# Optimization experiments

Measured on AMD Instinct MI355X. Metric: run time of the kernel, lower is better.

## Reference

```python
import jax, jax.numpy as jnp
import numpy as np

# LoFTR coarse-matching config (eval path, no padding masks)
THR = 0.2
BORDER_RM = 2
TEMP = 0.1
H0C, W0C = 60, 80  # L = 4800
H1C, W1C = 60, 80  # S = 4800
N, C = 2, 256


def _border_valid(h, w, bd):
    # flat [h*w] bool, False within bd of any border of the (h, w) grid
    hi = jnp.arange(h)
    wi = jnp.arange(w)
    vh = (hi >= bd) & (hi < h - bd)
    vw = (wi >= bd) & (wi < w - bd)
    return (vh[:, None] & vw[None, :]).reshape(-1)


def setup_inputs() -> dict:
    key = jax.random.key(0)
    k0, k1 = jax.random.split(key)
    feat_c0 = jax.random.normal(k0, (N, H0C * W0C, C), dtype=jnp.float32)
    feat_c1 = jax.random.normal(k1, (N, H1C * W1C, C), dtype=jnp.float32)
    return {"feat_c0": feat_c0, "feat_c1": feat_c1}


def reference(feat_c0, feat_c1):
    c = feat_c0.shape[-1]
    inv_sqrt_c = 1.0 / (float(c) ** 0.5)
    f0 = feat_c0 * inv_sqrt_c
    f1 = feat_c1 * inv_sqrt_c
    # [N, L, S] similarity
    sim = jnp.einsum('nlc,nsc->nls', f0, f1) / TEMP
    # dual softmax
    conf = jax.nn.softmax(sim, axis=1) * jax.nn.softmax(sim, axis=2)
    # threshold + border removal
    mask = conf > THR
    valid0 = _border_valid(H0C, W0C, BORDER_RM)  # [L]
    valid1 = _border_valid(H1C, W1C, BORDER_RM)  # [S]
    mask = mask & valid0[None, :, None] & valid1[None, None, :]
    # mutual nearest neighbour
    mask = mask \
        & (conf == jnp.max(conf, axis=2, keepdims=True)) \
        & (conf == jnp.max(conf, axis=1, keepdims=True))
    return conf, mask
```

## Files before the change

kernel.cpp:

```cpp
#include <hip/hip_runtime.h>
#include <hip/hip_bf16.h>
#include <cstdint>

static constexpr int   Nb = 2;
static constexpr int   L  = 4800;
static constexpr int   S  = 4800;
static constexpr int   C  = 256;
static constexpr float THR = 0.2f;
static constexpr float SIM_SCALE = 1.0f / 25.6f;
static constexpr unsigned CAND_CAP = 65536;

using f32x4  = __attribute__((ext_vector_type(4))) float;
using bf16x8 = __attribute__((ext_vector_type(8))) short;
using u32x4  = __attribute__((ext_vector_type(4))) unsigned int;

__device__ inline unsigned short bf16_rne(float x) {
    unsigned u = __float_as_uint(x);
    unsigned r = (u + 0x7FFFu + ((u >> 16) & 1u)) >> 16;
    return (unsigned short)r;
}

__global__ __launch_bounds__(256) void cvt_bf16(const float* __restrict__ in0,
                                                const float* __restrict__ in1,
                                                unsigned short* __restrict__ out0,
                                                unsigned short* __restrict__ out1,
                                                int n8,
                                                unsigned* __restrict__ stats, int nStats) {
    if (blockIdx.y == 0) {
        int si = blockIdx.x * 256 + threadIdx.x;
        if (si < nStats) stats[si] = 0u;
    }
    const float* in = blockIdx.y ? in1 : in0;
    unsigned short* out = blockIdx.y ? out1 : out0;
    int i = blockIdx.x * 256 + threadIdx.x;
    if (i >= n8) return;
    f32x4 a = *(const f32x4*)(in + (size_t)i * 8);
    f32x4 b = *(const f32x4*)(in + (size_t)i * 8 + 4);
    union { unsigned short us[8]; u32x4 v; } r;
#pragma unroll
    for (int j = 0; j < 4; j++) r.us[j] = bf16_rne(a[j]);
#pragma unroll
    for (int j = 0; j < 4; j++) r.us[4 + j] = bf16_rne(b[j]);
    *(u32x4*)(out + (size_t)i * 8) = r.v;
}

__device__ inline bool border_ok(int idx) {
    int h = idx / 80, w = idx % 80;
    return (h >= 2) & (h < 58) & (w >= 2) & (w < 78);
}

#define BM 96
#define BN 192
#define BK 64

static constexpr int NWG   = (L / BM) * (S / BN) * Nb;
static constexpr int TILE_X = S / BN;
static constexpr int TILES_PER_N = (L / BM) * TILE_X;
static constexpr int XQ = NWG / 8;
static constexpr int XR = NWG % 8;

__device__ inline void gload16(const void* g, void* l) {
    __builtin_amdgcn_global_load_lds(
        (const __attribute__((address_space(1))) unsigned int*)g,
        (__attribute__((address_space(3))) unsigned int*)l, 16, 0, 0);
}

template <int MODE>
__global__ __launch_bounds__(256) void gemm_pass(
    const unsigned short* __restrict__ Abf,
    const unsigned short* __restrict__ Bbf,
    float* __restrict__ rowSum,
    float* __restrict__ colSum,
    float* __restrict__ conf,
    float* __restrict__ mask,
    unsigned* __restrict__ rowMax,
    unsigned* __restrict__ colMax,
    unsigned* __restrict__ cnt,
    unsigned* __restrict__ cand)
{
    __shared__ unsigned short As[BM * BK];
    __shared__ unsigned short Bs[BN * BK];

    const int orig = blockIdx.x;
    const int xcd  = orig & 7;
    const int idx  = orig >> 3;
    const int wgid = (xcd < XR ? xcd * (XQ + 1) : XR * (XQ + 1) + (xcd - XR) * XQ) + idx;
    const int n    = wgid / TILES_PER_N;
    const int rem  = wgid % TILES_PER_N;
    const int rb   = (rem / TILE_X) * BM;
    const int cb   = (rem % TILE_X) * BN;

    const int t  = threadIdx.x;
    const int lane = t & 63;
    const int wid  = t >> 6;
    const int wr = wid >> 1, wc = wid & 1;

    const unsigned short* Ag = Abf + ((size_t)n * L + rb) * C;
    const unsigned short* Bg = Bbf + ((size_t)n * S + cb) * C;

    f32x4 acc[3][6] = {};

    for (int kt = 0; kt < C; kt += BK) {
#pragma unroll
        for (int i = 0; i < 3; i++) {
            int ix = wid * 192 + i * 64 + lane;
            int row = ix >> 3;
            int src = ((ix & 7) ^ (row & 7)) * 8 + kt;
            gload16(Ag + (size_t)row * C + src, &As[(wid * 192 + i * 64) * 8]);
        }
#pragma unroll
        for (int i = 0; i < 6; i++) {
            int ix = wid * 384 + i * 64 + lane;
            int row = ix >> 3;
            int src = ((ix & 7) ^ (row & 7)) * 8 + kt;
            gload16(Bg + (size_t)row * C + src, &Bs[(wid * 384 + i * 64) * 8]);
        }
        __syncthreads();

#pragma unroll
        for (int kk = 0; kk < 2; kk++) {
            bf16x8 a[3], b[6];
            const int kElem = kk * 32 + (lane >> 4) * 8;
#pragma unroll
            for (int f = 0; f < 3; f++) {
                int ra = wr * 48 + f * 16 + (lane & 15);
                a[f] = *(const bf16x8*)&As[ra * 64 + (kElem ^ ((ra & 7) << 3))];
            }
#pragma unroll
            for (int f = 0; f < 6; f++) {
                int rbi = wc * 96 + f * 16 + (lane & 15);
                b[f] = *(const bf16x8*)&Bs[rbi * 64 + (kElem ^ ((rbi & 7) << 3))];
            }
#pragma unroll
            for (int fi = 0; fi < 3; fi++)
#pragma unroll
                for (int fj = 0; fj < 6; fj++)
                    acc[fi][fj] = __builtin_amdgcn_mfma_f32_16x16x32_bf16(
                        b[fj], a[fi], acc[fi][fj], 0, 0, 0);
        }
        __syncthreads();
    }

    const int rowBase = rb + wr * 48;
    const int colBase = cb + wc * 96;

    if constexpr (MODE == 0) {
        float csum[6][4] = {};
#pragma unroll
        for (int fi = 0; fi < 3; fi++) {
            const int l = rowBase + fi * 16 + (lane & 15);
            float rsum = 0.f;
#pragma unroll
            for (int fj = 0; fj < 6; fj++) {
#pragma unroll
                for (int r = 0; r < 4; r++) {
                    float e = __expf(acc[fi][fj][r] * SIM_SCALE);
                    rsum += e;
                    csum[fj][r] += e;
                }
            }
            rsum += __shfl_xor(rsum, 16);
            rsum += __shfl_xor(rsum, 32);
            if (lane < 16)
                atomicAdd(&rowSum[(size_t)n * L + l], rsum);
        }
#pragma unroll
        for (int fj = 0; fj < 6; fj++)
#pragma unroll
            for (int r = 0; r < 4; r++) {
                float v = csum[fj][r];
                v += __shfl_xor(v, 1);
                v += __shfl_xor(v, 2);
                v += __shfl_xor(v, 4);
                v += __shfl_xor(v, 8);
                if ((lane & 15) == 0)
                    atomicAdd(&colSum[(size_t)n * S + colBase + fj * 16 + ((lane >> 4) << 2) + r], v);
            }
        const f32x4 zero4 = {0.f, 0.f, 0.f, 0.f};
        const size_t mbase = (size_t)wgid * 18432;
#pragma unroll
        for (int i = 0; i < 18; i++)
            *(f32x4*)&mask[mbase + ((size_t)i * 256 + t) * 4] = zero4;
    } else {
        f32x4 invD1[6];
#pragma unroll
        for (int fj = 0; fj < 6; fj++) {
            const int s0 = colBase + fj * 16 + ((lane >> 4) << 2);
            f32x4 d1 = *(const f32x4*)&colSum[(size_t)n * S + s0];
#pragma unroll
            for (int j = 0; j < 4; j++) invD1[fj][j] = 1.0f / d1[j];
        }
        float cmax[6][4] = {};

#pragma unroll
        for (int fi = 0; fi < 3; fi++) {
            const int l = rowBase + fi * 16 + (lane & 15);
            const float invD2 = 1.0f / rowSum[(size_t)n * L + l];
            const bool bl = border_ok(l);
            float rmax = 0.f;
#pragma unroll
            for (int fj = 0; fj < 6; fj++) {
                const int s0 = colBase + fj * 16 + ((lane >> 4) << 2);
                f32x4 cv;
#pragma unroll
                for (int r = 0; r < 4; r++) {
                    float e = __expf(acc[fi][fj][r] * SIM_SCALE);
                    float c = e * e * invD1[fj][r] * invD2;
                    cv[r] = c;
                    rmax = fmaxf(rmax, c);
                    cmax[fj][r] = fmaxf(cmax[fj][r], c);
                    if (c > THR) {
                        int s = s0 + r;
                        if (bl && border_ok(s)) {
                            unsigned pos = atomicAdd(cnt, 1u);
                            if (pos < CAND_CAP) {
                                cand[2 * pos]     = (unsigned)(((size_t)n * L + l) * S + s);
                                cand[2 * pos + 1] = __float_as_uint(c);
                            }
                        }
                    }
                }
                *(f32x4*)&conf[((size_t)n * L + l) * S + s0] = cv;
            }
            rmax = fmaxf(rmax, __shfl_xor(rmax, 16));
            rmax = fmaxf(rmax, __shfl_xor(rmax, 32));
            if (lane < 16)
                atomicMax(&rowMax[(size_t)n * L + l], __float_as_uint(rmax));
        }
#pragma unroll
        for (int fj = 0; fj < 6; fj++)
#pragma unroll
            for (int r = 0; r < 4; r++) {
                float v = cmax[fj][r];
                v = fmaxf(v, __shfl_xor(v, 1));
                v = fmaxf(v, __shfl_xor(v, 2));
                v = fmaxf(v, __shfl_xor(v, 4));
                v = fmaxf(v, __shfl_xor(v, 8));
                if ((lane & 15) == 0)
                    atomicMax(&colMax[(size_t)n * S + colBase + fj * 16 + ((lane >> 4) << 2) + r],
                              __float_as_uint(v));
            }
    }
}

__global__ __launch_bounds__(256) void mask_scatter(
    const unsigned* __restrict__ cnt,
    const unsigned* __restrict__ cand,
    const unsigned* __restrict__ rowMax,
    const unsigned* __restrict__ colMax,
    float* __restrict__ mask)
{
    unsigned nc = *cnt;
    if (nc > CAND_CAP) nc = CAND_CAP;
    for (unsigned i = blockIdx.x * 256 + threadIdx.x; i < nc; i += gridDim.x * 256) {
        unsigned flat = cand[2 * i];
        unsigned bits = cand[2 * i + 1];
        unsigned row = flat / S;
        unsigned s   = flat % S;
        unsigned n   = row / L;
        if (bits == rowMax[row] && bits == colMax[n * S + s])
            mask[flat] = 1.0f;
    }
}

extern "C" void kernel_launch(void* const* d_in, const int* in_sizes, int n_in,
                              void* d_out, int out_size, void* d_ws, size_t ws_size,
                              hipStream_t stream) {
    (void)in_sizes; (void)n_in; (void)out_size; (void)ws_size;
    const float* f0 = (const float*)d_in[0];
    const float* f1 = (const float*)d_in[1];

    float* conf = (float*)d_out;
    float* mask = conf + (size_t)Nb * L * S;

    unsigned short* Abf = (unsigned short*)d_ws;
    unsigned short* Bbf = Abf + (size_t)Nb * L * C;
    float* rowSum = (float*)(Bbf + (size_t)Nb * S * C);
    float* colSum = rowSum + (size_t)Nb * L;
    unsigned* rowMax = (unsigned*)(colSum + (size_t)Nb * S);
    unsigned* colMax = rowMax + (size_t)Nb * L;
    unsigned* cnt    = colMax + (size_t)Nb * S;
    unsigned* cand   = cnt + 2;

    const int nStats = 2 * (Nb * L + Nb * S) + 1;
    const int n8 = Nb * L * C / 8;
    cvt_bf16<<<dim3((n8 + 255) / 256, 2), 256, 0, stream>>>(f0, f1, Abf, Bbf, n8,
                                                            (unsigned*)rowSum, nStats);

    gemm_pass<0><<<NWG, 256, 0, stream>>>(Abf, Bbf, rowSum, colSum,
                                          nullptr, mask, nullptr, nullptr, nullptr, nullptr);
    gemm_pass<1><<<NWG, 256, 0, stream>>>(Abf, Bbf, rowSum, colSum,
                                          conf, nullptr, rowMax, colMax, cnt, cand);

    mask_scatter<<<32, 256, 0, stream>>>(cnt, cand, rowMax, colMax, mask);
}
```

Baseline: 161.9 us.

## Keep full-K A tile resident in LDS and process five column tiles per block

Each workgroup now loads its whole 96x256 A row tile into LDS once and then loops over five consecutive 192-wide B column tiles, reusing A instead of reloading it per tile. The grid shrinks by a factor of five and launch bounds request two blocks per CU. The aim is to cut A global loads and per-block launch overhead. The cost is more LDS per block, fewer blocks to spread across CUs (a possible tail imbalance), and longer serial work per block with no overlap between tiles.

```diff
diff --git a/kernel.cpp b/kernel.cpp
--- a/kernel.cpp
+++ b/kernel.cpp
@@ -16,8 +16,7 @@
 
 __device__ inline unsigned short bf16_rne(float x) {
     unsigned u = __float_as_uint(x);
-    unsigned r = (u + 0x7FFFu + ((u >> 16) & 1u)) >> 16;
-    return (unsigned short)r;
+    return (unsigned short)((u + 0x7FFFu + ((u >> 16) & 1u)) >> 16);
 }
 
 __global__ __launch_bounds__(256) void cvt_bf16(const float* __restrict__ in0,
@@ -53,11 +52,14 @@
 #define BN 192
 #define BK 64
 
-static constexpr int NWG   = (L / BM) * (S / BN) * Nb;
+static constexpr int NT     = C / BK;
+static constexpr int TPBLK  = 5;
 static constexpr int TILE_X = S / BN;
 static constexpr int TILES_PER_N = (L / BM) * TILE_X;
-static constexpr int XQ = NWG / 8;
-static constexpr int XR = NWG % 8;
+static constexpr int NTILES = TILES_PER_N * Nb;
+static constexpr int NBLK   = NTILES / TPBLK;
+static constexpr int XQ = NBLK / 8;
+static constexpr int XR = NBLK % 8;
 
 __device__ inline void gload16(const void* g, void* l) {
     __builtin_amdgcn_global_load_lds(
@@ -66,7 +68,7 @@
 }
 
 template <int MODE>
-__global__ __launch_bounds__(256) void gemm_pass(
+__global__ __launch_bounds__(256, 2) void gemm_pass(
     const unsigned short* __restrict__ Abf,
     const unsigned short* __restrict__ Bbf,
     float* __restrict__ rowSum,
@@ -78,17 +80,19 @@
     unsigned* __restrict__ cnt,
     unsigned* __restrict__ cand)
 {
-    __shared__ unsigned short As[BM * BK];
-    __shared__ unsigned short Bs[BN * BK];
+    __shared__ __align__(16) unsigned short As[BM * C];
+    __shared__ __align__(16) unsigned short Bs[BN * BK];
 
     const int orig = blockIdx.x;
     const int xcd  = orig & 7;
     const int idx  = orig >> 3;
-    const int wgid = (xcd < XR ? xcd * (XQ + 1) : XR * (XQ + 1) + (xcd - XR) * XQ) + idx;
-    const int n    = wgid / TILES_PER_N;
-    const int rem  = wgid % TILES_PER_N;
-    const int rb   = (rem / TILE_X) * BM;
-    const int cb   = (rem % TILE_X) * BN;
+    const int gb   = (xcd < XR ? xcd * (XQ + 1) : XR * (XQ + 1) + (xcd - XR) * XQ) + idx;
+
+    const int wg0  = gb * TPBLK;
+    const int n    = wg0 / TILES_PER_N;
+    const int rem0 = wg0 % TILES_PER_N;
+    const int rb   = (rem0 / TILE_X) * BM;
+    const int cb0  = (rem0 % TILE_X) * BN;
 
     const int t  = threadIdx.x;
     const int lane = t & 63;
@@ -96,150 +100,160 @@
     const int wr = wid >> 1, wc = wid & 1;
 
     const unsigned short* Ag = Abf + ((size_t)n * L + rb) * C;
-    const unsigned short* Bg = Bbf + ((size_t)n * S + cb) * C;
-
-    f32x4 acc[3][6] = {};
-
-    for (int kt = 0; kt < C; kt += BK) {
-#pragma unroll
-        for (int i = 0; i < 3; i++) {
-            int ix = wid * 192 + i * 64 + lane;
-            int row = ix >> 3;
-            int src = ((ix & 7) ^ (row & 7)) * 8 + kt;
-            gload16(Ag + (size_t)row * C + src, &As[(wid * 192 + i * 64) * 8]);
+
+#pragma unroll
+    for (int i = 0; i < 12; i++) {
+        int ix  = i * 256 + t;
+        int row = ix >> 5;
+        int c16 = ix & 31;
+        int src = ((c16 & 24) | ((c16 & 7) ^ (row & 7))) * 8;
+        gload16(Ag + (size_t)row * C + src, &As[ix * 8]);
+    }
+
+#pragma unroll 1
+    for (int ti = 0; ti < TPBLK; ++ti) {
+        const int wgid = wg0 + ti;
+        const int cb   = cb0 + ti * BN;
+        const unsigned short* Bg = Bbf + ((size_t)n * S + cb) * C;
+
+        f32x4 acc[3][6] = {};
+
+#pragma unroll
+        for (int kt = 0; kt < NT; ++kt) {
+#pragma unroll
+            for (int i = 0; i < 6; i++) {
+                int ix  = wid * 384 + i * 64 + lane;
+                int row = ix >> 3;
+                int src = ((ix & 7) ^ (row & 7)) * 8 + kt * BK;
+                gload16(Bg + (size_t)row * C + src, &Bs[(wid * 384 + i * 64) * 8]);
+            }
+            __syncthreads();
+
+#pragma unroll
+            for (int kk = 0; kk < 2; kk++) {
+                bf16x8 a[3], b[6];
+                const int gkA = kt * BK + kk * 32 + (lane >> 4) * 8;
+                const int kEB = kk * 32 + (lane >> 4) * 8;
+#pragma unroll
+                for (int f = 0; f < 3; f++) {
+                    int ra = wr * 48 + f * 16 + (lane & 15);
+                    a[f] = *(const bf16x8*)&As[ra * 256 + (gkA ^ ((ra & 7) << 3))];
+                }
+#pragma unroll
+                for (int f = 0; f < 6; f++) {
+                    int rbi = wc * 96 + f * 16 + (lane & 15);
+                    b[f] = *(const bf16x8*)&Bs[rbi * 64 + (kEB ^ ((rbi & 7) << 3))];
+                }
+#pragma unroll
+                for (int fi = 0; fi < 3; fi++)
+#pragma unroll
+                    for (int fj = 0; fj < 6; fj++)
+                        acc[fi][fj] = __builtin_amdgcn_mfma_f32_16x16x32_bf16(
+                            b[fj], a[fi], acc[fi][fj], 0, 0, 0);
+            }
+            __syncthreads();
         }
-#pragma unroll
-        for (int i = 0; i < 6; i++) {
-            int ix = wid * 384 + i * 64 + lane;
-            int row = ix >> 3;
-            int src = ((ix & 7) ^ (row & 7)) * 8 + kt;
-            gload16(Bg + (size_t)row * C + src, &Bs[(wid * 384 + i * 64) * 8]);
-        }
-        __syncthreads();
-
-#pragma unroll
-        for (int kk = 0; kk < 2; kk++) {
-            bf16x8 a[3], b[6];
-            const int kElem = kk * 32 + (lane >> 4) * 8;
-#pragma unroll
-            for (int f = 0; f < 3; f++) {
-                int ra = wr * 48 + f * 16 + (lane & 15);
-                a[f] = *(const bf16x8*)&As[ra * 64 + (kElem ^ ((ra & 7) << 3))];
-            }
-#pragma unroll
-            for (int f = 0; f < 6; f++) {
-                int rbi = wc * 96 + f * 16 + (lane & 15);
-                b[f] = *(const bf16x8*)&Bs[rbi * 64 + (kElem ^ ((rbi & 7) << 3))];
-            }
-#pragma unroll
-            for (int fi = 0; fi < 3; fi++)
-#pragma unroll
-                for (int fj = 0; fj < 6; fj++)
-                    acc[fi][fj] = __builtin_amdgcn_mfma_f32_16x16x32_bf16(
-                        b[fj], a[fi], acc[fi][fj], 0, 0, 0);
-        }
-        __syncthreads();
-    }
-
-    const int rowBase = rb + wr * 48;
-    const int colBase = cb + wc * 96;
-
-    if constexpr (MODE == 0) {
-        float csum[6][4] = {};
-#pragma unroll
-        for (int fi = 0; fi < 3; fi++) {
-            const int l = rowBase + fi * 16 + (lane & 15);
-            float rsum = 0.f;
-#pragma unroll
-            for (int fj = 0; fj < 6; fj++) {
+
+        const int rowBase = rb + wr * 48;
+        const int colBase = cb + wc * 96;
+
+        if constexpr (MODE == 0) {
+            float csum[6][4] = {};
+#pragma unroll
+            for (int fi = 0; fi < 3; fi++) {
+                const int l = rowBase + fi * 16 + (lane & 15);
+                float rsum = 0.f;
+#pragma unroll
+                for (int fj = 0; fj < 6; fj++) {
+#pragma unroll
+                    for (int r = 0; r < 4; r++) {
+                        float e = __expf(acc[fi][fj][r] * SIM_SCALE);
+                        rsum += e;
+                        csum[fj][r] += e;
+                    }
+                }
+                rsum += __shfl_xor(rsum, 16);
+                rsum += __shfl_xor(rsum, 32);
+                if (lane < 16)
+                    atomicAdd(&rowSum[(size_t)n * L + l], rsum);
+            }
+#pragma unroll
+            for (int fj = 0; fj < 6; fj++)
 #pragma unroll
                 for (int r = 0; r < 4; r++) {
-                    float e = __expf(acc[fi][fj][r] * SIM_SCALE);
-                    rsum += e;
-                    csum[fj][r] += e;
-                }
-            }
-            rsum += __shfl_xor(rsum, 16);
-            rsum += __shfl_xor(rsum, 32);
-            if (lane < 16)
-                atomicAdd(&rowSum[(size_t)n * L + l], rsum);
-        }
-#pragma unroll
-        for (int fj = 0; fj < 6; fj++)
-#pragma unroll
-            for (int r = 0; r < 4; r++) {
-                float v = csum[fj][r];
-                v += __shfl_xor(v, 1);
-                v += __shfl_xor(v, 2);
-                v += __shfl_xor(v, 4);
-                v += __shfl_xor(v, 8);
-                if ((lane & 15) == 0)
-                    atomicAdd(&colSum[(size_t)n * S + colBase + fj * 16 + ((lane >> 4) << 2) + r], v);
-            }
-        const f32x4 zero4 = {0.f, 0.f, 0.f, 0.f};
-        const size_t mbase = (size_t)wgid * 18432;
-#pragma unroll
-        for (int i = 0; i < 18; i++)
-            *(f32x4*)&mask[mbase + ((size_t)i * 256 + t) * 4] = zero4;
-    } else {
-        f32x4 invD1[6];
-#pragma unroll
-        for (int fj = 0; fj < 6; fj++) {
-            const int s0 = colBase + fj * 16 + ((lane >> 4) << 2);
-            f32x4 d1 = *(const f32x4*)&colSum[(size_t)n * S + s0];
-#pragma unroll
-            for (int j = 0; j < 4; j++) invD1[fj][j] = 1.0f / d1[j];
-        }
-        float cmax[6][4] = {};
-
-#pragma unroll
-        for (int fi = 0; fi < 3; fi++) {
-            const int l = rowBase + fi * 16 + (lane & 15);
-            const float invD2 = 1.0f / rowSum[(size_t)n * L + l];
-            const bool bl = border_ok(l);
-            float rmax = 0.f;
+                    float v = csum[fj][r];
+                    v += __shfl_xor(v, 1);
+                    v += __shfl_xor(v, 2);
+                    v += __shfl_xor(v, 4);
+                    v += __shfl_xor(v, 8);
+                    if ((lane & 15) == 0)
+                        atomicAdd(&colSum[(size_t)n * S + colBase + fj * 16 + ((lane >> 4) << 2) + r], v);
+                }
+            const f32x4 zero4 = {0.f, 0.f, 0.f, 0.f};
+            const size_t mbase = (size_t)wgid * 18432;
+#pragma unroll
+            for (int i = 0; i < 18; i++)
+                *(f32x4*)&mask[mbase + ((size_t)i * 256 + t) * 4] = zero4;
+        } else {
+            f32x4 invD1[6];
 #pragma unroll
             for (int fj = 0; fj < 6; fj++) {
                 const int s0 = colBase + fj * 16 + ((lane >> 4) << 2);
-                f32x4 cv;
-#pragma unroll
-                for (int r = 0; r < 4; r++) {
-                    float e = __expf(acc[fi][fj][r] * SIM_SCALE);
-                    float c = e * e * invD1[fj][r] * invD2;
-                    cv[r] = c;
-                    rmax = fmaxf(rmax, c);
-                    cmax[fj][r] = fmaxf(cmax[fj][r], c);
-                    if (c > THR) {
-                        int s = s0 + r;
-                        if (bl && border_ok(s)) {
-                            unsigned pos = atomicAdd(cnt, 1u);
-                            if (pos < CAND_CAP) {
-                                cand[2 * pos]     = (unsigned)(((size_t)n * L + l) * S + s);
-                                cand[2 * pos + 1] = __float_as_uint(c);
+                f32x4 d1 = *(const f32x4*)&colSum[(size_t)n * S + s0];
+#pragma unroll
+                for (int j = 0; j < 4; j++) invD1[fj][j] = 1.0f / d1[j];
+            }
+            float cmax[6][4] = {};
+
+#pragma unroll
+            for (int fi = 0; fi < 3; fi++) {
+                const int l = rowBase + fi * 16 + (lane & 15);
+                const float invD2 = 1.0f / rowSum[(size_t)n * L + l];
+                const bool bl = border_ok(l);
+                float rmax = 0.f;
+#pragma unroll
+                for (int fj = 0; fj < 6; fj++) {
+                    const int s0 = colBase + fj * 16 + ((lane >> 4) << 2);
+                    f32x4 cv;
+#pragma unroll
+                    for (int r = 0; r < 4; r++) {
+                        float e = __expf(acc[fi][fj][r] * SIM_SCALE);
+                        float c = e * e * invD1[fj][r] * invD2;
+                        cv[r] = c;
+                        rmax = fmaxf(rmax, c);
+                        cmax[fj][r] = fmaxf(cmax[fj][r], c);
+                        if (c > THR) {
+                            int s = s0 + r;
+                            if (bl && border_ok(s)) {
+                                unsigned pos = atomicAdd(cnt, 1u);
+                                if (pos < CAND_CAP) {
+                                    cand[2 * pos]     = (unsigned)(((size_t)n * L + l) * S + s);
+                                    cand[2 * pos + 1] = __float_as_uint(c);
+                                }
                             }
                         }
                     }
-                }
-                *(f32x4*)&conf[((size_t)n * L + l) * S + s0] = cv;
-            }
-            rmax = fmaxf(rmax, __shfl_xor(rmax, 16));
-            rmax = fmaxf(rmax, __shfl_xor(rmax, 32));
-            if (lane < 16)
-                atomicMax(&rowMax[(size_t)n * L + l], __float_as_uint(rmax));
+                    *(f32x4*)&conf[((size_t)n * L + l) * S + s0] = cv;
+                }
+                rmax = fmaxf(rmax, __shfl_xor(rmax, 16));
+                rmax = fmaxf(rmax, __shfl_xor(rmax, 32));
+                if (lane < 16)
+                    atomicMax(&rowMax[(size_t)n * L + l], __float_as_uint(rmax));
+            }
+#pragma unroll
+            for (int fj = 0; fj < 6; fj++)
+#pragma unroll
+                for (int r = 0; r < 4; r++) {
+                    float v = cmax[fj][r];
+                    v = fmaxf(v, __shfl_xor(v, 1));
+                    v = fmaxf(v, __shfl_xor(v, 2));
+                    v = fmaxf(v, __shfl_xor(v, 4));
+                    v = fmaxf(v, __shfl_xor(v, 8));
+                    if ((lane & 15) == 0)
+                        atomicMax(&colMax[(size_t)n * S + colBase + fj * 16 + ((lane >> 4) << 2) + r],
+                                  __float_as_uint(v));
+                }
         }
-#pragma unroll
-        for (int fj = 0; fj < 6; fj++)
-#pragma unroll
-            for (int r = 0; r < 4; r++) {
-                float v = cmax[fj][r];
-                v = fmaxf(v, __shfl_xor(v, 1));
-                v = fmaxf(v, __shfl_xor(v, 2));
-                v = fmaxf(v, __shfl_xor(v, 4));
-                v = fmaxf(v, __shfl_xor(v, 8));
-                if ((lane & 15) == 0)
-                    atomicMax(&colMax[(size_t)n * S + colBase + fj * 16 + ((lane >> 4) << 2) + r],
-                              __float_as_uint(v));
-            }
     }
 }
 
@@ -280,17 +294,17 @@
     unsigned* rowMax = (unsigned*)(colSum + (size_t)Nb * S);
     unsigned* colMax = rowMax + (size_t)Nb * L;
     unsigned* cnt    = colMax + (size_t)Nb * S;
-    unsigned* cand   = cnt + 2;
-
-    const int nStats = 2 * (Nb * L + Nb * S) + 1;
+    unsigned* cand   = cnt + 4;
+
+    const int nStats = 2 * (Nb * L + Nb * S) + 4;
     const int n8 = Nb * L * C / 8;
     cvt_bf16<<<dim3((n8 + 255) / 256, 2), 256, 0, stream>>>(f0, f1, Abf, Bbf, n8,
                                                             (unsigned*)rowSum, nStats);
 
-    gemm_pass<0><<<NWG, 256, 0, stream>>>(Abf, Bbf, rowSum, colSum,
-                                          nullptr, mask, nullptr, nullptr, nullptr, nullptr);
-    gemm_pass<1><<<NWG, 256, 0, stream>>>(Abf, Bbf, rowSum, colSum,
-                                          conf, nullptr, rowMax, colMax, cnt, cand);
+    gemm_pass<0><<<NBLK, 256, 0, stream>>>(Abf, Bbf, rowSum, colSum,
+                                           nullptr, mask, nullptr, nullptr, nullptr, nullptr);
+    gemm_pass<1><<<NBLK, 256, 0, stream>>>(Abf, Bbf, rowSum, colSum,
+                                           conf, nullptr, rowMax, colMax, cnt, cand);
 
     mask_scatter<<<32, 256, 0, stream>>>(cnt, cand, rowMax, colMax, mask);
 }
```

New measurement: 208.0 us. 28.5% more time.
